# Kernel optimization log

Hardware: AMD Instinct MI355X
Metric: run time of the kernel (lower is better)

Reference implementation:

```python
import jax, jax.numpy as jnp
import numpy as np

B, S, H = 8, 8192, 1024
CAPACITY_FACTOR = 0.5


def setup_inputs() -> dict:
    key = jax.random.key(0)
    ks = jax.random.split(key, 5)
    sc = lambda fan: np.float32(1.0 / np.sqrt(fan))
    return {
        "x": jax.random.normal(ks[0], (B, S, H), dtype=jnp.float32),
        # router: Linear(H, H//4) -> ReLU -> Linear(H//4, 1)
        "W1": jax.random.normal(ks[1], (H, H // 4), dtype=jnp.float32) * sc(H),
        "b1": jnp.zeros((H // 4,), dtype=jnp.float32),
        "W2": jax.random.normal(ks[2], (H // 4, 1), dtype=jnp.float32) * sc(H // 4),
        "b2": jnp.zeros((1,), dtype=jnp.float32),
        # external layer_fn realized as a dense layer: gelu(x @ Wl)
        "Wl": jax.random.normal(ks[3], (H, H), dtype=jnp.float32) * sc(H),
    }


def reference(x, W1, b1, W2, b2, Wl):
    # router scores [B, S, 1]
    scores = jax.nn.relu(jnp.einsum("bsh,hd->bsd", x, W1) + b1)
    scores = jnp.einsum("bsd,do->bso", scores, W2) + b2
    routing_weights = jax.nn.sigmoid(scores)  # [B, S, 1]

    # eval path: process only top-capacity tokens per batch row
    capacity = int(S * CAPACITY_FACTOR)
    _, top_idx = jax.lax.top_k(scores[..., 0], capacity)  # [B, C]

    selected = jnp.take_along_axis(x, top_idx[..., None], axis=1)  # [B, C, H]
    processed = jax.nn.gelu(jnp.einsum("bch,hd->bcd", selected, Wl))  # layer_fn

    batch_idx = jnp.arange(x.shape[0])[:, None]  # [B, 1]
    output = x.at[batch_idx, top_idx].set(processed)  # scatter back into clone of x
    return output, routing_weights
```

## Files before the change

### kernel.cpp

```cpp
#include <hip/hip_runtime.h>
#include <stdint.h>

#define B_   8
#define S_   8192
#define H_   1024
#define HQ_  256
#define CAP_ 4096
#define UCAP_ (S_-CAP_)
#define M_   (B_*CAP_)
#define EPSB 5e-3f
#define LCAP 8192

using f32x4 = __attribute__((ext_vector_type(4))) float;
using s16x8 = __attribute__((ext_vector_type(8))) short;

__device__ __forceinline__ unsigned short f2bf(float f) {
  unsigned u = __float_as_uint(f);
  u += 0x7FFF + ((u >> 16) & 1);
  return (unsigned short)(u >> 16);
}
__device__ __forceinline__ float bf2f(unsigned short h) {
  return __uint_as_float(((unsigned)h) << 16);
}

__device__ __forceinline__ float gelu_f(float v) {
  float s = v + 0.044715f * v * v * v;
  float e = __expf(-1.5957691216057308f * s);
  return v * __builtin_amdgcn_rcpf(1.0f + e);
}

__device__ __forceinline__ unsigned mono(float f) {
  unsigned u = __float_as_uint(f);
  return (u & 0x80000000u) ? ~u : (u | 0x80000000u);
}
__device__ __forceinline__ float unmono(unsigned k) {
  unsigned u = (k & 0x80000000u) ? (k & 0x7fffffffu) : ~k;
  return __uint_as_float(u);
}

__device__ __forceinline__ void gload_lds16(const void* g, void* l) {
  __builtin_amdgcn_global_load_lds(
      (const __attribute__((address_space(1))) void*)(uintptr_t)g,
      (__attribute__((address_space(3))) void*)(uintptr_t)l,
      16, 0, 0);
}

__global__ __launch_bounds__(256) void prep_w1_kernel(
    const float* __restrict__ W1, unsigned short* __restrict__ w1t_hi,
    unsigned short* __restrict__ w1t_lo) {
  __shared__ float tile[32][33];
  const int n0 = blockIdx.x * 32, k0 = blockIdx.y * 32;
  const int tx = threadIdx.x, ty = threadIdx.y;
  for (int i = ty; i < 32; i += 8) tile[i][tx] = W1[(size_t)(k0 + i) * HQ_ + n0 + tx];
  __syncthreads();
  for (int i = ty; i < 32; i += 8) {
    float v = tile[tx][i];
    unsigned short h = f2bf(v);
    w1t_hi[(size_t)(n0 + i) * H_ + k0 + tx] = h;
    w1t_lo[(size_t)(n0 + i) * H_ + k0 + tx] = f2bf(v - bf2f(h));
  }
}

__global__ __launch_bounds__(512) void router_mfma_kernel(
    const float* __restrict__ x, const unsigned short* __restrict__ w1t_hi,
    const unsigned short* __restrict__ w1t_lo, const float* __restrict__ b1,
    const float* __restrict__ W2, const float* __restrict__ b2,
    float* __restrict__ scores) {
  __shared__ __align__(16) unsigned short AsH[128 * 32];
  __shared__ __align__(16) unsigned short BsH[256 * 32];
  __shared__ __align__(16) unsigned short BsL[256 * 32];
  __shared__ float part[128][4];
  const int t = threadIdx.x;
  const int lane = t & 63, w = t >> 6;
  const int m0 = blockIdx.x * 128;
  const int wr = w >> 2, wc = w & 3;
  const int r16 = lane & 15, ks = lane >> 4;

  f32x4 acc[4][4];
  #pragma unroll
  for (int i = 0; i < 4; ++i)
    #pragma unroll
    for (int j = 0; j < 4; ++j) acc[i][j] = (f32x4){0.f, 0.f, 0.f, 0.f};

  for (int k0 = 0; k0 < H_; k0 += 32) {
    #pragma unroll
    for (int u = 0; u < 2; ++u) {
      int idx = t + u * 512;
      int row = idx >> 3, q = idx & 7;
      float4 v = *(const float4*)&x[(size_t)(m0 + row) * H_ + k0 + q * 4];
      ushort4 hh;
      hh.x = f2bf(v.x); hh.y = f2bf(v.y); hh.z = f2bf(v.z); hh.w = f2bf(v.w);
      int so = row * 32 + (((q >> 1) ^ (row & 3)) << 3) + (q & 1) * 4;
      *(ushort4*)&AsH[so] = hh;
    }
    #pragma unroll
    for (int q = 0; q < 2; ++q) {
      int c0 = (q * 8 + w) * 64;
      int g = c0 + lane;
      int row = g >> 2, sl = g & 3;
      int slz = sl ^ (row & 3);
      gload_lds16(&w1t_hi[(size_t)row * H_ + k0 + slz * 8], &BsH[c0 * 8]);
      gload_lds16(&w1t_lo[(size_t)row * H_ + k0 + slz * 8], &BsL[c0 * 8]);
    }
    __syncthreads();
    s16x8 ah[4], bh[4], bl[4];
    #pragma unroll
    for (int i = 0; i < 4; ++i) {
      int r = wr * 64 + i * 16 + r16;
      int co = (ks ^ (r & 3)) * 8;
      ah[i] = *(const s16x8*)&AsH[r * 32 + co];
    }
    #pragma unroll
    for (int j = 0; j < 4; ++j) {
      int r = wc * 64 + j * 16 + r16;
      int co = (ks ^ (r & 3)) * 8;
      bh[j] = *(const s16x8*)&BsH[r * 32 + co];
      bl[j] = *(const s16x8*)&BsL[r * 32 + co];
    }
    #pragma unroll
    for (int i = 0; i < 4; ++i)
      #pragma unroll
      for (int j = 0; j < 4; ++j) {
        acc[i][j] = __builtin_amdgcn_mfma_f32_16x16x32_bf16(ah[i], bh[j], acc[i][j], 0, 0, 0);
        acc[i][j] = __builtin_amdgcn_mfma_f32_16x16x32_bf16(ah[i], bl[j], acc[i][j], 0, 0, 0);
      }
    __syncthreads();
  }

  float b1v[4], w2v[4];
  #pragma unroll
  for (int j = 0; j < 4; ++j) {
    int n = wc * 64 + j * 16 + r16;
    b1v[j] = b1[n]; w2v[j] = W2[n];
  }
  const int g4 = lane >> 4;
  #pragma unroll
  for (int i = 0; i < 4; ++i) {
    #pragma unroll
    for (int r = 0; r < 4; ++r) {
      float p = 0.f;
      #pragma unroll
      for (int j = 0; j < 4; ++j) {
        float h = acc[i][j][r] + b1v[j];
        h = fmaxf(h, 0.f);
        p = fmaf(h, w2v[j], p);
      }
      p += __shfl_xor(p, 1);
      p += __shfl_xor(p, 2);
      p += __shfl_xor(p, 4);
      p += __shfl_xor(p, 8);
      if (r16 == 0) part[wr * 64 + i * 16 + g4 * 4 + r][wc] = p;
    }
  }
  __syncthreads();
  if (t < 128)
    scores[m0 + t] = part[t][0] + part[t][1] + part[t][2] + part[t][3] + b2[0];
}

__global__ __launch_bounds__(1024) void select_kernel(
    const float* __restrict__ scores, float* __restrict__ thr) {
  __shared__ unsigned hist[2048];
  __shared__ unsigned sh_b, sh_gt;
  const int b = blockIdx.x;
  const int tid = threadIdx.x;
  const float* srow = scores + (size_t)b * S_;
  unsigned prefix = 0; int plen = 0; unsigned rank = CAP_;
  #pragma unroll
  for (int round = 0; round < 3; ++round) {
    const int nb = (round < 2) ? 11 : 10;
    hist[tid] = 0; hist[tid + 1024] = 0;
    __syncthreads();
    for (int i = tid; i < S_; i += 1024) {
      unsigned k = mono(srow[i]);
      if (plen == 0 || (k >> (32 - plen)) == prefix) {
        unsigned bucket = (k << plen) >> (32 - nb);
        atomicAdd(&hist[bucket], 1u);
      }
    }
    __syncthreads();
    for (int s = 1; s < 2048; s <<= 1) {
      unsigned t0 = (tid + s < 2048) ? hist[tid + s] : 0;
      unsigned t1 = (tid + 1024 + s < 2048) ? hist[tid + 1024 + s] : 0;
      __syncthreads();
      hist[tid] += t0; hist[tid + 1024] += t1;
      __syncthreads();
    }
    #pragma unroll
    for (int h = 0; h < 2; ++h) {
      int i = tid + h * 1024;
      unsigned ge = hist[i];
      unsigned gt = (i < 2047) ? hist[i + 1] : 0;
      if (gt < rank && rank <= ge) { sh_b = (unsigned)i; sh_gt = gt; }
    }
    __syncthreads();
    prefix = (prefix << nb) | sh_b;
    plen += nb;
    rank -= sh_gt;
    __syncthreads();
  }
  if (tid == 0) thr[b] = unmono(prefix);
}

__global__ __launch_bounds__(256) void band_kernel(
    const float* __restrict__ scores, const float* __restrict__ thr,
    int* __restrict__ list, int* __restrict__ count) {
  int i = blockIdx.x * 256 + threadIdx.x;
  float s = scores[i];
  int b = i >> 13;
  if (fabsf(s - thr[b]) <= EPSB) {
    int p = atomicAdd(count, 1);
    if (p < LCAP) list[p] = i;
  }
}

__global__ __launch_bounds__(256) void recompute_kernel(
    const float* __restrict__ x, const float* __restrict__ W1,
    const float* __restrict__ b1, const float* __restrict__ W2,
    const float* __restrict__ b2, const int* __restrict__ list,
    const int* __restrict__ count, float* __restrict__ scores) {
  __shared__ float xr[4][H_];
  __shared__ float red[4][4];
  int n = *count; if (n > LCAP) n = LCAP;
  const int j = threadIdx.x;
  for (int base = blockIdx.x * 4; base < n; base += gridDim.x * 4) {
    int nt = n - base; if (nt > 4) nt = 4;
    for (int tt = 0; tt < 4; ++tt) {
      int tok = list[base + ((tt < nt) ? tt : 0)];
      const float* xrow = x + (size_t)tok * H_;
      for (int k = j; k < H_; k += 256) xr[tt][k] = xrow[k];
    }
    __syncthreads();
    float a0 = 0.f, a1 = 0.f, a2 = 0.f, a3 = 0.f;
    for (int k = 0; k < H_; ++k) {
      float wv = W1[(size_t)k * HQ_ + j];
      a0 = fmaf(xr[0][k], wv, a0);
      a1 = fmaf(xr[1][k], wv, a1);
      a2 = fmaf(xr[2][k], wv, a2);
      a3 = fmaf(xr[3][k], wv, a3);
    }
    float aa[4] = {a0, a1, a2, a3};
    #pragma unroll
    for (int tt = 0; tt < 4; ++tt) {
      float h = fmaxf(aa[tt] + b1[j], 0.f);
      float v = h * W2[j];
      v += __shfl_xor(v, 1);  v += __shfl_xor(v, 2);  v += __shfl_xor(v, 4);
      v += __shfl_xor(v, 8);  v += __shfl_xor(v, 16); v += __shfl_xor(v, 32);
      if ((j & 63) == 0) red[tt][j >> 6] = v;
    }
    __syncthreads();
    if (j < nt)
      scores[list[base + j]] = red[j][0] + red[j][1] + red[j][2] + red[j][3] + b2[0];
    __syncthreads();
  }
}

__global__ __launch_bounds__(1024) void compact_kernel(
    const float* __restrict__ scores, const float* __restrict__ thr,
    int* __restrict__ comp, int* __restrict__ ucomp) {
  __shared__ int wc_eq[16], wc_sel[16], red[16];
  const int b = blockIdx.x;
  const float T = thr[b];
  const float* srow = scores + (size_t)b * S_;
  const int tid = threadIdx.x, lane = tid & 63, wid = tid >> 6;

  int cgt = 0;
  #pragma unroll
  for (int c = 0; c < 8; ++c) cgt += (srow[c * 1024 + tid] > T) ? 1 : 0;
  cgt += __shfl_xor(cgt, 1);  cgt += __shfl_xor(cgt, 2);  cgt += __shfl_xor(cgt, 4);
  cgt += __shfl_xor(cgt, 8);  cgt += __shfl_xor(cgt, 16); cgt += __shfl_xor(cgt, 32);
  if (lane == 0) red[wid] = cgt;
  __syncthreads();
  int cnt_gt = 0;
  #pragma unroll
  for (int i = 0; i < 16; ++i) cnt_gt += red[i];
  const int need = CAP_ - cnt_gt;

  int* crow = comp + b * CAP_;
  int* urow = ucomp + b * UCAP_;
  int sel_base = 0, unsel_base = 0, eq_base = 0;
  __syncthreads();
  for (int c = 0; c < 8; ++c) {
    int idx = c * 1024 + tid;
    float s = srow[idx];
    bool gt = s > T, eq = (s == T);
    unsigned long long meq = __ballot(eq);
    if (lane == 0) wc_eq[wid] = __popcll(meq);
    __syncthreads();
    int eq_off = eq_base, eq_tot = 0;
    #pragma unroll
    for (int w2 = 0; w2 < 16; ++w2) { if (w2 < wid) eq_off += wc_eq[w2]; eq_tot += wc_eq[w2]; }
    int eqpos = eq_off + __popcll(meq & ((1ull << lane) - 1));
    bool take = gt || (eq && eqpos < need);
    unsigned long long mt = __ballot(take);
    if (lane == 0) wc_sel[wid] = __popcll(mt);
    __syncthreads();
    int sel_off = sel_base, sel_tot = 0;
    #pragma unroll
    for (int w2 = 0; w2 < 16; ++w2) { if (w2 < wid) sel_off += wc_sel[w2]; sel_tot += wc_sel[w2]; }
    if (take) {
      crow[sel_off + __popcll(mt & ((1ull << lane) - 1))] = idx;
    } else {
      int un_off = unsel_base + wid * 64 - (sel_off - sel_base);
      urow[un_off + __popcll(~mt & ((1ull << lane) - 1))] = idx;
    }
    sel_base += sel_tot; unsel_base += 1024 - sel_tot; eq_base += eq_tot;
    __syncthreads();
  }
}

__global__ __launch_bounds__(256) void rw_kernel(
    const float* __restrict__ scores, float* __restrict__ rw) {
  int i = blockIdx.x * 256 + threadIdx.x;
  rw[i] = 1.f / (1.f + expf(-scores[i]));
}

__global__ __launch_bounds__(256) void copy_unsel_kernel(
    const float* __restrict__ x, const int* __restrict__ ucomp,
    float* __restrict__ out) {
  int i = blockIdx.x;
  int b = i >> 12, r = i & (UCAP_ - 1);
  int token = ucomp[b * UCAP_ + r];
  size_t row = (size_t)b * S_ + token;
  const float4* src = (const float4*)(x + row * H_);
  float4* dst = (float4*)(out + row * H_);
  dst[threadIdx.x] = src[threadIdx.x];
}

__global__ __launch_bounds__(256) void wlt_kernel(
    const float* __restrict__ wl, unsigned short* __restrict__ wlt) {
  __shared__ float tile[32][33];
  const int x0 = blockIdx.x * 32, y0 = blockIdx.y * 32;
  const int tx = threadIdx.x, ty = threadIdx.y;
  for (int i = ty; i < 32; i += 8) tile[i][tx] = wl[(size_t)(y0 + i) * H_ + x0 + tx];
  __syncthreads();
  for (int i = ty; i < 32; i += 8)
    wlt[(size_t)(x0 + i) * H_ + y0 + tx] = f2bf(tile[tx][i]);
}

__global__ __launch_bounds__(256) void gather_cast_kernel(
    const float* __restrict__ x, const int* __restrict__ comp,
    unsigned short* __restrict__ xg) {
  int tid = blockIdx.x * 256 + threadIdx.x;
  int rowc = tid >> 8;
  int c4 = tid & 255;
  int b = rowc >> 12, cc = rowc & (CAP_ - 1);
  int token = comp[b * CAP_ + cc];
  float4 v = *(const float4*)&x[((size_t)(b * S_ + token)) * H_ + c4 * 4];
  ushort4 o;
  o.x = f2bf(v.x); o.y = f2bf(v.y); o.z = f2bf(v.z); o.w = f2bf(v.w);
  *(ushort4*)&xg[(size_t)rowc * H_ + c4 * 4] = o;
}

__global__ __launch_bounds__(256) void moe_gemm_kernel(
    const unsigned short* __restrict__ xg, const unsigned short* __restrict__ wlt,
    const int* __restrict__ comp, float* __restrict__ out) {
  __shared__ __align__(16) unsigned short As[128 * 64];
  __shared__ __align__(16) unsigned short Bs[128 * 64];
  __shared__ int toks[128];
  const int t = threadIdx.x;
  const int lane = t & 63, w = t >> 6;
  const int bid = blockIdx.x;
  const int xcd = bid & 7, wl_ = bid >> 3;
  const int m0 = (xcd * 32 + (wl_ >> 3)) * 128;
  const int n0 = (wl_ & 7) * 128;
  const int bb = m0 >> 12;
  if (t < 128) toks[t] = comp[bb * CAP_ + (m0 & (CAP_ - 1)) + t];
  const int wr = w >> 1, wc = w & 1;
  const int r16 = lane & 15, ks = lane >> 4;

  const unsigned short* aS[4];
  const unsigned short* bS[4];
  #pragma unroll
  for (int u = 0; u < 4; ++u) {
    int c = u * 256 + t;
    int row = c >> 3, sl = c & 7;
    int slz = sl ^ (row & 7);
    aS[u] = xg + (size_t)(m0 + row) * H_ + slz * 8;
    bS[u] = wlt + (size_t)(n0 + row) * H_ + slz * 8;
  }

  f32x4 acc[4][4];
  #pragma unroll
  for (int i = 0; i < 4; ++i)
    #pragma unroll
    for (int j = 0; j < 4; ++j) acc[i][j] = (f32x4){0.f, 0.f, 0.f, 0.f};

  for (int k0 = 0; k0 < H_; k0 += 64) {
    #pragma unroll
    for (int u = 0; u < 4; ++u) {
      gload_lds16(aS[u] + k0, &As[(u * 256 + w * 64) * 8]);
      gload_lds16(bS[u] + k0, &Bs[(u * 256 + w * 64) * 8]);
    }
    __syncthreads();
    #pragma unroll
    for (int kk = 0; kk < 2; ++kk) {
      s16x8 af[4], bfr[4];
      const int g = kk * 4 + ks;
      #pragma unroll
      for (int i = 0; i < 4; ++i) {
        int r = wr * 64 + i * 16 + r16;
        af[i] = *(const s16x8*)&As[r * 64 + (g ^ (r & 7)) * 8];
      }
      #pragma unroll
      for (int j = 0; j < 4; ++j) {
        int r = wc * 64 + j * 16 + r16;
        bfr[j] = *(const s16x8*)&Bs[r * 64 + (g ^ (r & 7)) * 8];
      }
      #pragma unroll
      for (int i = 0; i < 4; ++i)
        #pragma unroll
        for (int j = 0; j < 4; ++j)
          acc[i][j] = __builtin_amdgcn_mfma_f32_16x16x32_bf16(af[i], bfr[j], acc[i][j], 0, 0, 0);
    }
    __syncthreads();
  }

  #pragma unroll
  for (int i = 0; i < 4; ++i) {
    #pragma unroll
    for (int r = 0; r < 4; ++r) {
      int rl = wr * 64 + i * 16 + (lane >> 4) * 4 + r;
      int token = toks[rl];
      float* orow = out + ((size_t)(bb * S_ + token)) * H_ + n0 + wc * 64;
      #pragma unroll
      for (int j = 0; j < 4; ++j)
        orow[j * 16 + r16] = gelu_f(acc[i][j][r]);
    }
  }
}

extern "C" void kernel_launch(void* const* d_in, const int* in_sizes, int n_in,
                              void* d_out, int out_size, void* d_ws, size_t ws_size,
                              hipStream_t stream) {
  const float* x  = (const float*)d_in[0];
  const float* W1 = (const float*)d_in[1];
  const float* b1 = (const float*)d_in[2];
  const float* W2 = (const float*)d_in[3];
  const float* b2 = (const float*)d_in[4];
  const float* Wl = (const float*)d_in[5];
  float* out = (float*)d_out;
  float* rw  = out + (size_t)B_ * S_ * H_;

  char* ws = (char*)d_ws;
  float* scores        = (float*)ws;
  int*   comp          = (int*)(ws + (256 << 10));
  float* thr           = (float*)(ws + (384 << 10));
  int*   count         = (int*)(ws + (384 << 10) + 256);
  int*   list          = (int*)(ws + (384 << 10) + 512);
  int*   ucomp         = (int*)(ws + (448 << 10));
  unsigned short* wlt  = (unsigned short*)(ws + (1 << 20));
  unsigned short* xg   = (unsigned short*)(ws + (3 << 20));
  unsigned short* w1t_hi = xg;
  unsigned short* w1t_lo = xg + 262144;

  hipMemsetAsync(count, 0, sizeof(int), stream);
  hipLaunchKernelGGL(prep_w1_kernel, dim3(HQ_/32, H_/32), dim3(32, 8), 0, stream,
                     W1, w1t_hi, w1t_lo);
  hipLaunchKernelGGL(router_mfma_kernel, dim3((B_*S_)/128), dim3(512), 0, stream,
                     x, w1t_hi, w1t_lo, b1, W2, b2, scores);
  hipLaunchKernelGGL(select_kernel, dim3(B_), dim3(1024), 0, stream, scores, thr);
  hipLaunchKernelGGL(band_kernel, dim3((B_*S_)/256), dim3(256), 0, stream,
                     scores, thr, list, count);
  hipLaunchKernelGGL(recompute_kernel, dim3(128), dim3(256), 0, stream,
                     x, W1, b1, W2, b2, list, count, scores);
  hipLaunchKernelGGL(select_kernel, dim3(B_), dim3(1024), 0, stream, scores, thr);
  hipLaunchKernelGGL(compact_kernel, dim3(B_), dim3(1024), 0, stream,
                     scores, thr, comp, ucomp);
  hipLaunchKernelGGL(rw_kernel, dim3((B_*S_)/256), dim3(256), 0, stream,
                     scores, rw);
  hipLaunchKernelGGL(copy_unsel_kernel, dim3(B_*UCAP_), dim3(256), 0, stream,
                     x, ucomp, out);
  hipLaunchKernelGGL(wlt_kernel, dim3(H_/32, H_/32), dim3(32, 8), 0, stream, Wl, wlt);
  hipLaunchKernelGGL(gather_cast_kernel, dim3(M_*H_/4/256), dim3(256), 0, stream,
                     x, comp, xg);
  hipLaunchKernelGGL(moe_gemm_kernel, dim3((M_/128)*(H_/128)), dim3(256), 0, stream,
                     xg, wlt, comp, out);
}
```

Before: 417.2 us.

## Fuse gather-and-cast into MoE GEMM A-load and retile router to 64 rows

Removes the separate gather_cast kernel and its bf16 staging buffer; the GEMM now loads selected fp32 x rows directly via token indices, converts to bf16 in registers and writes swizzled LDS. This avoids writing and re-reading the gathered matrix but makes each n-block re-read fp32 rows and replaces async LDS loads with register staging. The router kernel is also retiled to 64-row blocks of 256 threads, each wave covering 64 of the hidden columns.

```diff
diff --git a/kernel.cpp b/kernel.cpp
--- a/kernel.cpp
+++ b/kernel.cpp
@@ -61,19 +61,18 @@
   }
 }
 
-__global__ __launch_bounds__(512) void router_mfma_kernel(
+__global__ __launch_bounds__(256) void router_mfma_kernel(
     const float* __restrict__ x, const unsigned short* __restrict__ w1t_hi,
     const unsigned short* __restrict__ w1t_lo, const float* __restrict__ b1,
     const float* __restrict__ W2, const float* __restrict__ b2,
     float* __restrict__ scores) {
-  __shared__ __align__(16) unsigned short AsH[128 * 32];
+  __shared__ __align__(16) unsigned short AsH[64 * 32];
   __shared__ __align__(16) unsigned short BsH[256 * 32];
   __shared__ __align__(16) unsigned short BsL[256 * 32];
-  __shared__ float part[128][4];
+  __shared__ float part[64][4];
   const int t = threadIdx.x;
   const int lane = t & 63, w = t >> 6;
-  const int m0 = blockIdx.x * 128;
-  const int wr = w >> 2, wc = w & 3;
+  const int m0 = blockIdx.x * 64;
   const int r16 = lane & 15, ks = lane >> 4;
 
   f32x4 acc[4][4];
@@ -85,7 +84,7 @@
   for (int k0 = 0; k0 < H_; k0 += 32) {
     #pragma unroll
     for (int u = 0; u < 2; ++u) {
-      int idx = t + u * 512;
+      int idx = t + u * 256;
       int row = idx >> 3, q = idx & 7;
       float4 v = *(const float4*)&x[(size_t)(m0 + row) * H_ + k0 + q * 4];
       ushort4 hh;
@@ -94,8 +93,8 @@
       *(ushort4*)&AsH[so] = hh;
     }
     #pragma unroll
-    for (int q = 0; q < 2; ++q) {
-      int c0 = (q * 8 + w) * 64;
+    for (int q = 0; q < 4; ++q) {
+      int c0 = (q * 4 + w) * 64;
       int g = c0 + lane;
       int row = g >> 2, sl = g & 3;
       int slz = sl ^ (row & 3);
@@ -106,13 +105,13 @@
     s16x8 ah[4], bh[4], bl[4];
     #pragma unroll
     for (int i = 0; i < 4; ++i) {
-      int r = wr * 64 + i * 16 + r16;
+      int r = i * 16 + r16;
       int co = (ks ^ (r & 3)) * 8;
       ah[i] = *(const s16x8*)&AsH[r * 32 + co];
     }
     #pragma unroll
     for (int j = 0; j < 4; ++j) {
-      int r = wc * 64 + j * 16 + r16;
+      int r = w * 64 + j * 16 + r16;
       int co = (ks ^ (r & 3)) * 8;
       bh[j] = *(const s16x8*)&BsH[r * 32 + co];
       bl[j] = *(const s16x8*)&BsL[r * 32 + co];
@@ -130,7 +129,7 @@
   float b1v[4], w2v[4];
   #pragma unroll
   for (int j = 0; j < 4; ++j) {
-    int n = wc * 64 + j * 16 + r16;
+    int n = w * 64 + j * 16 + r16;
     b1v[j] = b1[n]; w2v[j] = W2[n];
   }
   const int g4 = lane >> 4;
@@ -149,11 +148,11 @@
       p += __shfl_xor(p, 2);
       p += __shfl_xor(p, 4);
       p += __shfl_xor(p, 8);
-      if (r16 == 0) part[wr * 64 + i * 16 + g4 * 4 + r][wc] = p;
-    }
-  }
-  __syncthreads();
-  if (t < 128)
+      if (r16 == 0) part[i * 16 + g4 * 4 + r][w] = p;
+    }
+  }
+  __syncthreads();
+  if (t < 64)
     scores[m0 + t] = part[t][0] + part[t][1] + part[t][2] + part[t][3] + b2[0];
 }
 
@@ -337,22 +336,8 @@
     wlt[(size_t)(x0 + i) * H_ + y0 + tx] = f2bf(tile[tx][i]);
 }
 
-__global__ __launch_bounds__(256) void gather_cast_kernel(
-    const float* __restrict__ x, const int* __restrict__ comp,
-    unsigned short* __restrict__ xg) {
-  int tid = blockIdx.x * 256 + threadIdx.x;
-  int rowc = tid >> 8;
-  int c4 = tid & 255;
-  int b = rowc >> 12, cc = rowc & (CAP_ - 1);
-  int token = comp[b * CAP_ + cc];
-  float4 v = *(const float4*)&x[((size_t)(b * S_ + token)) * H_ + c4 * 4];
-  ushort4 o;
-  o.x = f2bf(v.x); o.y = f2bf(v.y); o.z = f2bf(v.z); o.w = f2bf(v.w);
-  *(ushort4*)&xg[(size_t)rowc * H_ + c4 * 4] = o;
-}
-
 __global__ __launch_bounds__(256) void moe_gemm_kernel(
-    const unsigned short* __restrict__ xg, const unsigned short* __restrict__ wlt,
+    const float* __restrict__ x, const unsigned short* __restrict__ wlt,
     const int* __restrict__ comp, float* __restrict__ out) {
   __shared__ __align__(16) unsigned short As[128 * 64];
   __shared__ __align__(16) unsigned short Bs[128 * 64];
@@ -368,16 +353,24 @@
   const int wr = w >> 1, wc = w & 1;
   const int r16 = lane & 15, ks = lane >> 4;
 
-  const unsigned short* aS[4];
   const unsigned short* bS[4];
   #pragma unroll
   for (int u = 0; u < 4; ++u) {
     int c = u * 256 + t;
     int row = c >> 3, sl = c & 7;
     int slz = sl ^ (row & 7);
-    aS[u] = xg + (size_t)(m0 + row) * H_ + slz * 8;
     bS[u] = wlt + (size_t)(n0 + row) * H_ + slz * 8;
   }
+  __syncthreads();
+  const float* aS[8];
+  int aOff[8];
+  #pragma unroll
+  for (int u = 0; u < 8; ++u) {
+    int idx = u * 256 + t;
+    int row = idx >> 4, c4 = idx & 15;
+    aS[u] = x + ((size_t)(bb * S_ + toks[row])) * H_ + c4 * 4;
+    aOff[u] = row * 64 + (((c4 >> 1) ^ (row & 7)) << 3) + (c4 & 1) * 4;
+  }
 
   f32x4 acc[4][4];
   #pragma unroll
@@ -386,10 +379,18 @@
     for (int j = 0; j < 4; ++j) acc[i][j] = (f32x4){0.f, 0.f, 0.f, 0.f};
 
   for (int k0 = 0; k0 < H_; k0 += 64) {
-    #pragma unroll
-    for (int u = 0; u < 4; ++u) {
-      gload_lds16(aS[u] + k0, &As[(u * 256 + w * 64) * 8]);
+    float4 av[8];
+    #pragma unroll
+    for (int u = 0; u < 8; ++u) av[u] = *(const float4*)(aS[u] + k0);
+    #pragma unroll
+    for (int u = 0; u < 4; ++u)
       gload_lds16(bS[u] + k0, &Bs[(u * 256 + w * 64) * 8]);
+    #pragma unroll
+    for (int u = 0; u < 8; ++u) {
+      ushort4 o;
+      o.x = f2bf(av[u].x); o.y = f2bf(av[u].y);
+      o.z = f2bf(av[u].z); o.w = f2bf(av[u].w);
+      *(ushort4*)&As[aOff[u]] = o;
     }
     __syncthreads();
     #pragma unroll
@@ -449,14 +450,13 @@
   int*   list          = (int*)(ws + (384 << 10) + 512);
   int*   ucomp         = (int*)(ws + (448 << 10));
   unsigned short* wlt  = (unsigned short*)(ws + (1 << 20));
-  unsigned short* xg   = (unsigned short*)(ws + (3 << 20));
-  unsigned short* w1t_hi = xg;
-  unsigned short* w1t_lo = xg + 262144;
+  unsigned short* w1t_hi = (unsigned short*)(ws + (3 << 20));
+  unsigned short* w1t_lo = w1t_hi + 262144;
 
   hipMemsetAsync(count, 0, sizeof(int), stream);
   hipLaunchKernelGGL(prep_w1_kernel, dim3(HQ_/32, H_/32), dim3(32, 8), 0, stream,
                      W1, w1t_hi, w1t_lo);
-  hipLaunchKernelGGL(router_mfma_kernel, dim3((B_*S_)/128), dim3(512), 0, stream,
+  hipLaunchKernelGGL(router_mfma_kernel, dim3((B_*S_)/64), dim3(256), 0, stream,
                      x, w1t_hi, w1t_lo, b1, W2, b2, scores);
   hipLaunchKernelGGL(select_kernel, dim3(B_), dim3(1024), 0, stream, scores, thr);
   hipLaunchKernelGGL(band_kernel, dim3((B_*S_)/256), dim3(256), 0, stream,
@@ -471,8 +471,6 @@
   hipLaunchKernelGGL(copy_unsel_kernel, dim3(B_*UCAP_), dim3(256), 0, stream,
                      x, ucomp, out);
   hipLaunchKernelGGL(wlt_kernel, dim3(H_/32, H_/32), dim3(32, 8), 0, stream, Wl, wlt);
-  hipLaunchKernelGGL(gather_cast_kernel, dim3(M_*H_/4/256), dim3(256), 0, stream,
-                     x, comp, xg);
   hipLaunchKernelGGL(moe_gemm_kernel, dim3((M_/128)*(H_/128)), dim3(256), 0, stream,
-                     xg, wlt, comp, out);
-}
+                     x, wlt, comp, out);
+}
```

Result: slower. 448.9 us (+7.6%).
